# Optimization experiments

Hardware: AMD Instinct MI355X
Metric: run time of the kernel (lower is better)

Reference implementation:

```python
import jax, jax.numpy as jnp
import numpy as np

B, N, D, H = 4, 1024, 1024, 16
DH = D // H  # 64
FF = 4 * D   # 4096


def _layernorm(x, w, b, eps=1e-5):
    mu = jnp.mean(x, axis=-1, keepdims=True)
    var = jnp.var(x, axis=-1, keepdims=True)
    return (x - mu) * jax.lax.rsqrt(var + eps) * w + b


def setup_inputs() -> dict:
    key = jax.random.key(0)
    ks = jax.random.split(key, 8)
    s = 0.02
    return {
        "x": jax.random.normal(ks[0], (B, N, D), jnp.float32),
        "ln1_w": jnp.ones((D,), jnp.float32),
        "ln1_b": jnp.zeros((D,), jnp.float32),
        "qkv_w": jax.random.normal(ks[1], (3 * D, D), jnp.float32) * s,
        "qkv_b": jnp.zeros((3 * D,), jnp.float32),
        "proj_l_w": jax.random.normal(ks[2], (H, H), jnp.float32) * s,
        "proj_l_b": jnp.zeros((H,), jnp.float32),
        "proj_w_w": jax.random.normal(ks[3], (H, H), jnp.float32) * s,
        "proj_w_b": jnp.zeros((H,), jnp.float32),
        "out_w": jax.random.normal(ks[4], (D, D), jnp.float32) * s,
        "out_b": jnp.zeros((D,), jnp.float32),
        "gamma1": jnp.ones((D,), jnp.float32),
        "ln2_w": jnp.ones((D,), jnp.float32),
        "ln2_b": jnp.zeros((D,), jnp.float32),
        "fc1_w": jax.random.normal(ks[5], (FF, D), jnp.float32) * s,
        "fc1_b": jnp.zeros((FF,), jnp.float32),
        "fc2_w": jax.random.normal(ks[6], (D, FF), jnp.float32) * s,
        "fc2_b": jnp.zeros((D,), jnp.float32),
        "gamma2": jnp.ones((D,), jnp.float32),
    }


def reference(x, ln1_w, ln1_b, qkv_w, qkv_b, proj_l_w, proj_l_b, proj_w_w,
              proj_w_b, out_w, out_b, gamma1, ln2_w, ln2_b, fc1_w, fc1_b,
              fc2_w, fc2_b, gamma2):
    # ---- LayerScale(TalkingHeadAttention) branch ----
    h = _layernorm(x, ln1_w, ln1_b)
    qkv = h @ qkv_w.T + qkv_b                      # [B,N,3D]
    q, k, v = jnp.split(qkv, 3, axis=-1)
    # [B,N,D] -> [B,H,N,DH]
    reshape = lambda t: t.reshape(B, N, H, DH).transpose(0, 2, 1, 3)
    q, k, v = reshape(q), reshape(k), reshape(v)
    attn = jnp.einsum("bhid,bhjd->bhij", q, k) * (DH ** -0.5)
    # talking-heads mixing before softmax (Linear over head dim)
    attn = jnp.einsum("bhij,gh->bgij", attn, proj_l_w) + proj_l_b[None, :, None, None]
    attn = jax.nn.softmax(attn, axis=-1)
    # talking-heads mixing after softmax
    attn = jnp.einsum("bhij,gh->bgij", attn, proj_w_w) + proj_w_b[None, :, None, None]
    o = jnp.einsum("bhij,bhjd->bhid", attn, v)     # [B,H,N,DH]
    o = o.transpose(0, 2, 1, 3).reshape(B, N, D)
    o = o @ out_w.T + out_b
    x = x + gamma1 * o
    # ---- LayerScale(MLP) branch ----
    h = _layernorm(x, ln2_w, ln2_b)
    h = jax.nn.gelu(h @ fc1_w.T + fc1_b)
    h = h @ fc2_w.T + fc2_b
    return x + gamma2 * h
```

## Files before the change

kernel.cpp:

```cpp
#include <hip/hip_runtime.h>


typedef _Float16 f16x8 __attribute__((ext_vector_type(8)));
typedef _Float16 f16x4 __attribute__((ext_vector_type(4)));
typedef _Float16 f16x2 __attribute__((ext_vector_type(2)));
typedef float f32x4 __attribute__((ext_vector_type(4)));

#define B_ 4
#define N_ 1024
#define D_ 1024
#define H_ 16
#define DH_ 64
#define FF_ 4096
#define M_ (B_ * N_)

__device__ __forceinline__ float gelu_act(float x) {
  float z = 0.7978845608028654f * (x + 0.044715f * x * x * x);
  return x / (1.0f + __expf(-2.0f * z));
}

__device__ __forceinline__ void ld_lds16(const _Float16* g, _Float16* l) {
  __builtin_amdgcn_global_load_lds((const __attribute__((address_space(1))) void*)g,
                                   (__attribute__((address_space(3))) void*)l, 16, 0, 0);
}

__device__ __forceinline__ int swz8(int i) {
  return (((i >> 2) << 1) ^ (i & 3)) & 7;
}
__device__ __forceinline__ int lds_off(int p, int i, int j) {
  int ch = ((j >> 3) ^ swz8(i) ^ ((p >> 2) << 1)) & 7;
  return p * 1032 + i * 64 + (ch << 3) + (j & 7);
}

__global__ __launch_bounds__(256) void cast_all(
    const float* __restrict__ a0, _Float16* __restrict__ o0,
    const float* __restrict__ a1, _Float16* __restrict__ o1,
    const float* __restrict__ a2, _Float16* __restrict__ o2,
    const float* __restrict__ a3, _Float16* __restrict__ o3,
    const float* __restrict__ W1, const float* __restrict__ W2,
    _Float16* __restrict__ w1f, _Float16* __restrict__ w2f,
    float* __restrict__ bsum,
    const float* __restrict__ x, const float* __restrict__ ln_w,
    const float* __restrict__ ln_b, _Float16* __restrict__ hb) {
  int b = blockIdx.x, t = threadIdx.x;
  if (b >= 12289) {
    int row = b - 12289;
    const float* xr = x + (size_t)row * D_;
    float4 v = *(const float4*)(xr + t * 4);
    float s = v.x + v.y + v.z + v.w;
    float sq = v.x * v.x + v.y * v.y + v.z * v.z + v.w * v.w;
    #pragma unroll
    for (int off = 32; off > 0; off >>= 1) {
      s += __shfl_down(s, off);
      sq += __shfl_down(sq, off);
    }
    __shared__ float red[8];
    int wave = t >> 6, lane = t & 63;
    if (lane == 0) { red[wave] = s; red[4 + wave] = sq; }
    __syncthreads();
    float ts = red[0] + red[1] + red[2] + red[3];
    float tq = red[4] + red[5] + red[6] + red[7];
    float mean = ts * (1.0f / (float)D_);
    float var = tq * (1.0f / (float)D_) - mean * mean;
    float rs = rsqrtf(var + 1e-5f);
    float4 wv = *(const float4*)(ln_w + t * 4);
    float4 bv = *(const float4*)(ln_b + t * 4);
    f16x4 o;
    o[0] = (_Float16)((v.x - mean) * rs * wv.x + bv.x);
    o[1] = (_Float16)((v.y - mean) * rs * wv.y + bv.y);
    o[2] = (_Float16)((v.z - mean) * rs * wv.z + bv.z);
    o[3] = (_Float16)((v.w - mean) * rs * wv.w + bv.w);
    *(f16x4*)(hb + (size_t)row * D_ + t * 4) = o;
    return;
  }
  const float* in;
  _Float16* out;
  int base;
  if (b < 3072) { in = a0; out = o0; base = b; }
  else if (b < 4096) { in = a1; out = o1; base = b - 3072; }
  else if (b < 8192) { in = a2; out = o2; base = b - 4096; }
  else if (b < 12288) { in = a3; out = o3; base = b - 8192; }
  else {
    w1f[t] = (_Float16)W1[t];
    w2f[t] = (_Float16)W2[t];
    float4 z = {0.f, 0.f, 0.f, 0.f};
    #pragma unroll
    for (int r = 0; r < 4; r++) *(float4*)(bsum + t * 16 + r * 4) = z;
    return;
  }
  int i = (base * 256 + t) * 4;
  float4 v = *(const float4*)(in + i);
  f16x4 o;
  o[0] = (_Float16)v.x; o[1] = (_Float16)v.y; o[2] = (_Float16)v.z; o[3] = (_Float16)v.w;
  *(f16x4*)(out + i) = o;
}

__global__ __launch_bounds__(256) void ln_f16(const float* __restrict__ x,
                                              const float* __restrict__ w,
                                              const float* __restrict__ b,
                                              _Float16* __restrict__ out) {
  int row = blockIdx.x;
  int tid = threadIdx.x;
  const float* xr = x + (size_t)row * D_;
  float4 v = *(const float4*)(xr + tid * 4);
  float s = v.x + v.y + v.z + v.w;
  float sq = v.x * v.x + v.y * v.y + v.z * v.z + v.w * v.w;
  #pragma unroll
  for (int off = 32; off > 0; off >>= 1) {
    s += __shfl_down(s, off);
    sq += __shfl_down(sq, off);
  }
  __shared__ float red[8];
  int wave = tid >> 6, lane = tid & 63;
  if (lane == 0) { red[wave] = s; red[4 + wave] = sq; }
  __syncthreads();
  float ts = red[0] + red[1] + red[2] + red[3];
  float tq = red[4] + red[5] + red[6] + red[7];
  float mean = ts * (1.0f / (float)D_);
  float var = tq * (1.0f / (float)D_) - mean * mean;
  float rs = rsqrtf(var + 1e-5f);
  float4 wv = *(const float4*)(w + tid * 4);
  float4 bv = *(const float4*)(b + tid * 4);
  f16x4 o;
  o[0] = (_Float16)((v.x - mean) * rs * wv.x + bv.x);
  o[1] = (_Float16)((v.y - mean) * rs * wv.y + bv.y);
  o[2] = (_Float16)((v.z - mean) * rs * wv.z + bv.z);
  o[3] = (_Float16)((v.w - mean) * rs * wv.w + bv.w);
  *(f16x4*)(out + (size_t)row * D_ + tid * 4) = o;
}

template <int EPI, int BN, int OCC, int SWAPXY>
__global__ __launch_bounds__(256, OCC) void gemm_nt(
    const _Float16* __restrict__ A, const _Float16* __restrict__ W,
    const float* __restrict__ bias, int M, int N, int K,
    _Float16* __restrict__ outB, float* __restrict__ outF,
    const float* __restrict__ res, const float* __restrict__ gamma) {
  __shared__ _Float16 As[128 * 64];
  __shared__ _Float16 Bs[BN * 64];
  int tid = threadIdx.x;
  int wave = tid >> 6, lane = tid & 63;
  int quad = lane >> 4, l16 = lane & 15;
  int wm = wave >> 1, wn = wave & 1;
  int m0 = (SWAPXY ? blockIdx.x : blockIdx.y) * 128;
  int n0 = (SWAPXY ? blockIdx.y : blockIdx.x) * BN;
  int lrow = lane >> 3, lcol = (lane & 7) * 8;
  const int NI = (BN == 128) ? 4 : 2;
  const int WN = (BN == 128) ? 64 : 32;

  f32x4 zero = {0.f, 0.f, 0.f, 0.f};
  f32x4 acc[4][NI];
  #pragma unroll
  for (int i = 0; i < 4; i++)
    #pragma unroll
    for (int j = 0; j < NI; j++) acc[i][j] = zero;

  for (int k0 = 0; k0 < K; k0 += 64) {
    __syncthreads();
    #pragma unroll
    for (int c = 0; c < 4; c++) {
      int rb = c * 32 + wave * 8;
      ld_lds16(A + (size_t)(m0 + rb + lrow) * K + k0 + lcol, As + rb * 64);
      if (BN == 128 || c < 2)
        ld_lds16(W + (size_t)(n0 + rb + lrow) * K + k0 + lcol, Bs + rb * 64);
    }
    __syncthreads();
    #pragma unroll
    for (int ks = 0; ks < 2; ks++) {
      int kk = ks * 32 + quad * 8;
      f16x8 a[4], bfr[NI];
      #pragma unroll
      for (int i = 0; i < 4; i++) a[i] = *(const f16x8*)(As + (wm * 64 + i * 16 + l16) * 64 + kk);
      #pragma unroll
      for (int i = 0; i < NI; i++) bfr[i] = *(const f16x8*)(Bs + (wn * WN + i * 16 + l16) * 64 + kk);
      #pragma unroll
      for (int mi = 0; mi < 4; mi++)
        #pragma unroll
        for (int ni = 0; ni < NI; ni++)
          acc[mi][ni] = __builtin_amdgcn_mfma_f32_16x16x32_f16(a[mi], bfr[ni], acc[mi][ni], 0, 0, 0);
    }
  }

  #pragma unroll
  for (int mi = 0; mi < 4; mi++) {
    int grow_base = m0 + wm * 64 + mi * 16 + quad * 4;
    #pragma unroll
    for (int ni = 0; ni < NI; ni++) {
      int gcol = n0 + wn * WN + ni * 16 + l16;
      float bb = bias[gcol];
      float gm = (EPI == 1) ? gamma[gcol] : 0.f;
      #pragma unroll
      for (int r = 0; r < 4; r++) {
        size_t oi = (size_t)(grow_base + r) * N + gcol;
        float c = acc[mi][ni][r] + bb;
        if (EPI == 0) {
          outB[oi] = (_Float16)c;
        } else if (EPI == 1) {
          outF[oi] = res[oi] + gm * c;
        } else {
          outB[oi] = (_Float16)gelu_act(c);
        }
      }
    }
  }
}

#define GPH_OPEN()                                      \
  __builtin_amdgcn_sched_barrier(0);                    \
  __builtin_amdgcn_s_barrier();                         \
  asm volatile("s_waitcnt lgkmcnt(0)" ::: "memory");    \
  __builtin_amdgcn_sched_barrier(0);                    \
  __builtin_amdgcn_s_setprio(1)

#define GPH_CLOSE()                                     \
  __builtin_amdgcn_s_setprio(0);                        \
  __builtin_amdgcn_sched_barrier(0);                    \
  __builtin_amdgcn_s_barrier()

#define GPH_CLOSE_VM(n)                                 \
  __builtin_amdgcn_s_setprio(0);                        \
  __builtin_amdgcn_sched_barrier(0);                    \
  asm volatile("s_waitcnt vmcnt(" #n ")" ::: "memory"); \
  __builtin_amdgcn_s_barrier()

#define GMFMA(MB, NB)                                                         \
  _Pragma("unroll") for (int ks = 0; ks < 2; ks++)                            \
  _Pragma("unroll") for (int mi = 0; mi < 4; mi++)                            \
  _Pragma("unroll") for (int ni = 0; ni < 2; ni++)                            \
    acc[MB + mi][NB + ni] = __builtin_amdgcn_mfma_f32_16x16x32_f16(           \
        ar[mi][ks], br[NB + ni][ks], acc[MB + mi][NB + ni], 0, 0, 0)

#define LDA(buf, MB)                                            \
  _Pragma("unroll") for (int ks = 0; ks < 2; ks++)              \
  _Pragma("unroll") for (int mi = 0; mi < 4; mi++)              \
    ar[mi][ks] = rdf(&lds[buf][0][wm][0], MB + mi, ks)

#define LDB(buf, NB)                                            \
  _Pragma("unroll") for (int ks = 0; ks < 2; ks++)              \
  _Pragma("unroll") for (int ni = 0; ni < 2; ni++)              \
    br[NB + ni][ks] = rdf(&lds[buf][1][wn >> 1][0], fbB + NB + ni, ks)

template <int EPI>
__global__ __launch_bounds__(512, 2) void gemm_nt8(
    const _Float16* __restrict__ A, const _Float16* __restrict__ W,
    const float* __restrict__ bias, int M, int N, int K,
    _Float16* __restrict__ outB, _Float16* __restrict__ outB2) {
  __shared__ _Float16 lds[2][2][2][8192];
  const int tid = threadIdx.x;
  const int wv = tid >> 6, lane = tid & 63;
  const int quad = lane >> 4, l16 = lane & 15;
  const int wm = wv >> 2, wn = wv & 3;
  const int fbB = (wn & 1) * 4;
  const int wg = ((int)blockIdx.x & 7) * ((int)gridDim.x >> 3) + ((int)blockIdx.x >> 3);
  int split = 0, kt0 = 0, m0, n0;
  if (EPI == 3) {
    split = wg >> 6;
    int rem = wg & 63;
    m0 = (rem & 15) << 8;
    n0 = (rem >> 4) << 8;
    kt0 = split << 4;
  } else {
    m0 = (wg & 15) << 8;
    n0 = (wg >> 4) << 8;
  }
  const int gc = ((lane & 7) ^ (lane >> 3)) << 3;
  const int srow = wv * 8 + (lane >> 3);

  auto stageA = [&](int lt, int h) {
    const _Float16* g = A + (size_t)(m0 + h * 128 + srow) * K + (kt0 + lt) * 64 + gc;
    _Float16* l = &lds[lt & 1][0][h][wv * 512];
    ld_lds16(g, l);
    ld_lds16(g + (size_t)64 * K, l + 4096);
  };
  auto stageB = [&](int lt, int h) {
    const _Float16* g = W + (size_t)(n0 + h * 128 + srow) * K + (kt0 + lt) * 64 + gc;
    _Float16* l = &lds[lt & 1][1][h][wv * 512];
    ld_lds16(g, l);
    ld_lds16(g + (size_t)64 * K, l + 4096);
  };
  auto rdf = [&](const _Float16* base, int fi, int ks) -> f16x8 {
    int row = fi * 16 + l16;
    int pc = ((ks << 2) + quad) ^ (l16 & 7);
    return *(const f16x8*)(base + row * 64 + (pc << 3));
  };

  f32x4 acc[8][4];
  const f32x4 zero = {0.f, 0.f, 0.f, 0.f};
  #pragma unroll
  for (int i = 0; i < 8; i++)
    #pragma unroll
    for (int j = 0; j < 4; j++) acc[i][j] = zero;
  f16x8 ar[4][2], br[4][2];

  stageA(0, 0); stageA(0, 1); stageB(0, 0); stageB(0, 1);
  stageB(1, 0); stageB(1, 1);
  asm volatile("s_waitcnt vmcnt(4)" ::: "memory");
  __builtin_amdgcn_s_barrier();

  const int NT = 16;
  const int ITERS = NT >> 1;
  for (int it = 0; it < ITERS - 1; ++it) {
    const int t0 = it * 2;
    LDA(0, 0); LDB(0, 0); stageA(t0 + 1, 0);
    GPH_OPEN(); GMFMA(0, 0); GPH_CLOSE();
    LDB(0, 2); stageA(t0 + 1, 1);
    GPH_OPEN(); GMFMA(0, 2); GPH_CLOSE();
    LDA(0, 4); stageB(t0 + 2, 0);
    GPH_OPEN(); GMFMA(4, 0); GPH_CLOSE();
    stageB(t0 + 2, 1);
    GPH_OPEN(); GMFMA(4, 2); GPH_CLOSE_VM(4);
    LDA(1, 0); LDB(1, 0); stageA(t0 + 2, 0);
    GPH_OPEN(); GMFMA(0, 0); GPH_CLOSE();
    LDB(1, 2); stageA(t0 + 2, 1);
    GPH_OPEN(); GMFMA(0, 2); GPH_CLOSE();
    LDA(1, 4); stageB(t0 + 3, 0);
    GPH_OPEN(); GMFMA(4, 0); GPH_CLOSE();
    stageB(t0 + 3, 1);
    GPH_OPEN(); GMFMA(4, 2); GPH_CLOSE_VM(4);
  }
  {
    LDA(0, 0); LDB(0, 0); stageA(NT - 1, 0);
    GPH_OPEN(); GMFMA(0, 0); GPH_CLOSE();
    LDB(0, 2); stageA(NT - 1, 1);
    GPH_OPEN(); GMFMA(0, 2); GPH_CLOSE();
    LDA(0, 4);
    GPH_OPEN(); GMFMA(4, 0); GPH_CLOSE();
    GPH_OPEN(); GMFMA(4, 2); GPH_CLOSE_VM(0);
    LDA(1, 0); LDB(1, 0);
    GPH_OPEN(); GMFMA(0, 0); GPH_CLOSE();
    LDB(1, 2);
    GPH_OPEN(); GMFMA(0, 2); GPH_CLOSE();
    LDA(1, 4);
    GPH_OPEN(); GMFMA(4, 0); GPH_CLOSE();
    GPH_OPEN(); GMFMA(4, 2); GPH_CLOSE();
  }

  _Float16* po = outB;
  if (EPI == 3)
    po = (split < 2 ? outB : outB2) + (size_t)(split & 1) * ((size_t)M * N);
  #pragma unroll
  for (int mi = 0; mi < 8; mi++) {
    int grow = m0 + wm * 128 + mi * 16 + quad * 4;
    #pragma unroll
    for (int ni = 0; ni < 4; ni++) {
      int gcol = n0 + wn * 64 + ni * 16 + l16;
      float bb = (EPI == 3) ? 0.f : bias[gcol];
      #pragma unroll
      for (int r = 0; r < 4; r++) {
        size_t oi = (size_t)(grow + r) * N + gcol;
        float c = acc[mi][ni][r] + bb;
        po[oi] = (_Float16)(EPI == 2 ? gelu_act(c) : c);
      }
    }
  }
}

__global__ __launch_bounds__(256) void fc2_combine(
    const _Float16* __restrict__ p01, const _Float16* __restrict__ p23,
    const float* __restrict__ x1, const float* __restrict__ gamma,
    const float* __restrict__ bias, float* __restrict__ out) {
  const size_t idx = ((size_t)blockIdx.x * 256 + threadIdx.x) * 4;
  const int col = (int)(idx & (D_ - 1));
  const size_t soff = (size_t)M_ * D_;
  f16x4 a = *(const f16x4*)(p01 + idx);
  f16x4 b = *(const f16x4*)(p01 + soff + idx);
  f16x4 c = *(const f16x4*)(p23 + idx);
  f16x4 d = *(const f16x4*)(p23 + soff + idx);
  float4 xv = *(const float4*)(x1 + idx);
  float4 gv = *(const float4*)(gamma + col);
  float4 bv = *(const float4*)(bias + col);
  float4 o;
  o.x = xv.x + gv.x * ((float)a[0] + (float)b[0] + (float)c[0] + (float)d[0] + bv.x);
  o.y = xv.y + gv.y * ((float)a[1] + (float)b[1] + (float)c[1] + (float)d[1] + bv.y);
  o.z = xv.z + gv.z * ((float)a[2] + (float)b[2] + (float)c[2] + (float)d[2] + bv.z);
  o.w = xv.w + gv.w * ((float)a[3] + (float)b[3] + (float)c[3] + (float)d[3] + bv.w);
  *(float4*)(out + idx) = o;
}

__global__ __launch_bounds__(256) void transpose_v(const _Float16* __restrict__ qkv,
                                                   _Float16* __restrict__ vt,
                                                   const float* __restrict__ b2,
                                                   float* __restrict__ bsum) {
  int jt = blockIdx.x;
  int h = blockIdx.y;
  int b = blockIdx.z;
  __shared__ _Float16 tl[64][68];
  int tid = threadIdx.x;
  int j0 = jt * 64;
  #pragma unroll
  for (int k = 0; k < 16; k++) {
    int idx = k * 256 + tid;
    int jr = idx >> 6, dc = idx & 63;
    tl[jr][dc] = qkv[(size_t)(b * N_ + j0 + jr) * (3 * D_) + 2 * D_ + h * 64 + dc];
  }
  __syncthreads();
  #pragma unroll
  for (int k = 0; k < 16; k++) {
    int idx = k * 256 + tid;
    int dr = idx >> 6, jc = idx & 63;
    vt[(size_t)((b * H_ + h) * DH_ + dr) * N_ + j0 + jc] = tl[jc][dr];
  }
  int d = tid & 63, jq = tid >> 6;
  float s = 0.f;
  #pragma unroll
  for (int r = 0; r < 16; r++) s += (float)tl[jq * 16 + r][d];
  atomicAdd(&bsum[b * D_ + h * 64 + d], b2[h] * s);
}

__global__ __launch_bounds__(1024, 4) void attn_th(
    const _Float16* __restrict__ qkv, const _Float16* __restrict__ vt,
    const _Float16* __restrict__ w1f, const _Float16* __restrict__ w2f,
    const float* __restrict__ b1f, const float* __restrict__ bsum,
    _Float16* __restrict__ ob) {
  __shared__ __align__(16) _Float16 SP[2 * 16512];
  __shared__ float lsum[272];
  _Float16* Sp = SP;
  _Float16* Pp = SP + 16512;

  const int tid = threadIdx.x;
  const int wave = tid >> 6;
  const int lane = tid & 63;
  const int quad = lane >> 4, l16 = lane & 15;
  const int i0 = blockIdx.y * 16;
  const int b = blockIdx.x;
  const size_t bN = (size_t)b * N_;
  const f32x4 zero = {0.f, 0.f, 0.f, 0.f};

  f16x8 qf[2];
  #pragma unroll
  for (int ks = 0; ks < 2; ks++) {
    f16x8 q = *(const f16x8*)(qkv + (bN + i0 + l16) * 3072 + wave * 64 + ks * 32 + quad * 8);
    #pragma unroll
    for (int e = 0; e < 8; e++) q[e] = q[e] * (_Float16)0.125f;
    qf[ks] = q;
  }
  f16x4 w1a = *(const f16x4*)(w1f + l16 * 16 + quad * 4);
  float b1v = b1f[l16];
  f32x4 b1i = {b1v, b1v, b1v, b1v};

  const _Float16* vbase = vt + (size_t)((b * H_ + wave) * DH_ + l16) * N_ + quad * 8;

  f32x4 uacc[4];
  #pragma unroll
  for (int nt = 0; nt < 4; nt++) uacc[nt] = zero;
  float lacc = 0.f;

  f16x8 kcur[4][2];
  auto loadK = [&](int j0) {
    #pragma unroll
    for (int jb = 0; jb < 4; jb++) {
      const _Float16* kb = qkv + (bN + j0 + jb * 16 + l16) * 3072 + 1024 + wave * 64 + quad * 8;
      kcur[jb][0] = *(const f16x8*)kb;
      kcur[jb][1] = *(const f16x8*)(kb + 32);
    }
  };
  loadK(0);

  f16x8 vreg[4];

  for (int t = 0; t < 16; t++) {
    int j0 = t * 64;
    f32x4 sres[4];
    #pragma unroll
    for (int jb = 0; jb < 4; jb++) {
      f32x4 s = __builtin_amdgcn_mfma_f32_16x16x32_f16(kcur[jb][0], qf[0], zero, 0, 0, 0);
      sres[jb] = __builtin_amdgcn_mfma_f32_16x16x32_f16(kcur[jb][1], qf[1], s, 0, 0, 0);
    }
    #pragma unroll
    for (int jb = 0; jb < 4; jb++) {
      f16x4 sv;
      #pragma unroll
      for (int r = 0; r < 4; r++) sv[r] = (_Float16)sres[jb][r];
      *(f16x4*)(Sp + lds_off(wave, l16, jb * 16 + quad * 4)) = sv;
    }
    if (t < 15) loadK(j0 + 64);
    #pragma unroll
    for (int nt = 0; nt < 4; nt++)
      vreg[nt] = *(const f16x8*)(vbase + (size_t)(nt * 16) * N_ + j0);
    __syncthreads();
    #pragma unroll
    for (int cg = 0; cg < 4; cg++) {
      f16x4 sf;
      #pragma unroll
      for (int t4 = 0; t4 < 4; t4++)
        sf[t4] = Sp[lds_off(quad * 4 + t4, wave, cg * 16 + l16)];
      f32x4 a = __builtin_amdgcn_mfma_f32_16x16x16f16(sf, w1a, b1i, 0, 0, 0);
      f16x4 pv;
      #pragma unroll
      for (int r = 0; r < 4; r++) {
        float e = __expf(a[r]);
        lacc += e;
        pv[r] = (_Float16)e;
      }
      *(f16x4*)(Pp + lds_off(l16, wave, cg * 16 + quad * 4)) = pv;
    }
    __syncthreads();
    f16x8 pf0 = *(const f16x8*)(Pp + lds_off(wave, l16, quad * 8));
    f16x8 pf1 = *(const f16x8*)(Pp + lds_off(wave, l16, 32 + quad * 8));
    #pragma unroll
    for (int nt = 0; nt < 4; nt++)
      uacc[nt] = __builtin_amdgcn_mfma_f32_16x16x32_f16(vreg[nt], pf0, uacc[nt], 0, 0, 0);
    #pragma unroll
    for (int nt = 0; nt < 4; nt++) {
      f16x8 vf = *(const f16x8*)(vbase + (size_t)(nt * 16) * N_ + j0 + 32);
      uacc[nt] = __builtin_amdgcn_mfma_f32_16x16x32_f16(vf, pf1, uacc[nt], 0, 0, 0);
    }
  }

  lacc += __shfl_xor(lacc, 16);
  lacc += __shfl_xor(lacc, 32);
  __syncthreads();
  if (quad == 0) lsum[l16 * 17 + wave] = lacc;
  __syncthreads();
  float invl = 1.0f / lsum[wave * 17 + l16];

  _Float16* Uf = Sp;
  #pragma unroll
  for (int nt = 0; nt < 4; nt++) {
    f16x4 u;
    #pragma unroll
    for (int r = 0; r < 4; r++) u[r] = (_Float16)(uacc[nt][r] * invl);
    *(f16x4*)(Uf + wave * 1092 + l16 * 68 + nt * 16 + quad * 4) = u;
  }
  __syncthreads();

  f16x4 w2a = *(const f16x4*)(w2f + l16 * 16 + quad * 4);
  #pragma unroll
  for (int cg = 0; cg < 4; cg++) {
    f16x4 af;
    #pragma unroll
    for (int t4 = 0; t4 < 4; t4++)
      af[t4] = Uf[(quad * 4 + t4) * 1092 + wave * 68 + cg * 16 + l16];
    f32x4 o = __builtin_amdgcn_mfma_f32_16x16x16f16(af, w2a, zero, 0, 0, 0);
    f32x4 bs = *(const f32x4*)(bsum + b * D_ + l16 * 64 + cg * 16 + quad * 4);
    f16x4 ov;
    #pragma unroll
    for (int r = 0; r < 4; r++) ov[r] = (_Float16)(o[r] + bs[r]);
    *(f16x4*)(ob + (bN + i0 + wave) * D_ + l16 * 64 + cg * 16 + quad * 4) = ov;
  }
}

extern "C" void kernel_launch(void* const* d_in, const int* in_sizes, int n_in,
                              void* d_out, int out_size, void* d_ws, size_t ws_size,
                              hipStream_t stream) {
  const float* x      = (const float*)d_in[0];
  const float* ln1_w  = (const float*)d_in[1];
  const float* ln1_b  = (const float*)d_in[2];
  const float* qkv_w  = (const float*)d_in[3];
  const float* qkv_b  = (const float*)d_in[4];
  const float* plw    = (const float*)d_in[5];
  const float* plb    = (const float*)d_in[6];
  const float* pww    = (const float*)d_in[7];
  const float* pwb    = (const float*)d_in[8];
  const float* out_w  = (const float*)d_in[9];
  const float* out_b  = (const float*)d_in[10];
  const float* gamma1 = (const float*)d_in[11];
  const float* ln2_w  = (const float*)d_in[12];
  const float* ln2_b  = (const float*)d_in[13];
  const float* fc1_w  = (const float*)d_in[14];
  const float* fc1_b  = (const float*)d_in[15];
  const float* fc2_w  = (const float*)d_in[16];
  const float* fc2_b  = (const float*)d_in[17];
  const float* gamma2 = (const float*)d_in[18];
  float* out = (float*)d_out;

  char* ws = (char*)d_ws;
  _Float16* wq   = (_Float16*)(ws + 0);
  _Float16* wo   = (_Float16*)(ws + 6291456);
  _Float16* wf1  = (_Float16*)(ws + 8388608);
  _Float16* wf2  = (_Float16*)(ws + 16777216);
  float*    x1   = (float*)   (ws + 25165824);
  _Float16* ob   = (_Float16*)(ws + 41943040);
  _Float16* hb   = (_Float16*)(ws + 50331648);
  _Float16* qkvb = (_Float16*)(ws + 58720256);
  _Float16* vtb  = (_Float16*)(ws + 83886080);
  _Float16* fb   = (_Float16*)(ws + 58720256);
  _Float16* w1f  = (_Float16*)(ws + 25165824);
  _Float16* w2f  = (_Float16*)(ws + 25165824 + 512);
  float*    bsum = (float*)   (ws + 25165824 + 1024);
  _Float16* p01  = (_Float16*)(ws + 0);
  _Float16* p23  = (_Float16*)(ws + 41943040);
  if (ws_size < 92274688) return;

  cast_all<<<16385, 256, 0, stream>>>(qkv_w, wq, out_w, wo, fc1_w, wf1, fc2_w, wf2,
                                      plw, pww, w1f, w2f, bsum,
                                      x, ln1_w, ln1_b, hb);

  gemm_nt8<0><<<192, 512, 0, stream>>>(hb, wq, qkv_b, M_, 3 * D_, D_, qkvb, nullptr);
  transpose_v<<<dim3(16, 16, 4), 256, 0, stream>>>(qkvb, vtb, pwb, bsum);
  attn_th<<<dim3(4, 64), 1024, 0, stream>>>(qkvb, vtb, w1f, w2f, plb, bsum, ob);
  gemm_nt<1, 128, 3, 1><<<dim3(32, 8), 256, 0, stream>>>(ob, wo, out_b, M_, D_, D_, nullptr, x1, x, gamma1);

  ln_f16<<<4096, 256, 0, stream>>>(x1, ln2_w, ln2_b, hb);
  gemm_nt8<2><<<256, 512, 0, stream>>>(hb, wf1, fc1_b, M_, FF_, D_, fb, nullptr);
  gemm_nt8<3><<<256, 512, 0, stream>>>(fb, wf2, fc2_b, M_, D_, FF_, p01, p23);
  fc2_combine<<<4096, 256, 0, stream>>>(p01, p23, x1, gamma2, fc2_b, out);
}
```

Baseline: 411.2 us.

## Overlap out/fc1/fc2 weight casts with QKV GEMM via extra blocks

The fp32→fp16 casts of the output-projection, fc1 and fc2 weights move out of the upfront cast kernel. They become 768 extra blocks appended to the QKV GEMM launch, so those casts run alongside the GEMM tiles on otherwise idle compute units instead of serialising before it. The pre-pass now only casts the QKV weight, the talking-head weights and runs LayerNorm1. The cost is that the GEMM kernel gains a branch and extra parameters, and the cast blocks compete with the GEMM tiles for memory bandwidth.

New measurement: 412.0 us, median of 2. Within noise of the previous version (+0.2%).

```diff
diff --git a/kernel.cpp b/kernel.cpp
--- a/kernel.cpp
+++ b/kernel.cpp
@@ -34,17 +34,14 @@
 
 __global__ __launch_bounds__(256) void cast_all(
     const float* __restrict__ a0, _Float16* __restrict__ o0,
-    const float* __restrict__ a1, _Float16* __restrict__ o1,
-    const float* __restrict__ a2, _Float16* __restrict__ o2,
-    const float* __restrict__ a3, _Float16* __restrict__ o3,
     const float* __restrict__ W1, const float* __restrict__ W2,
     _Float16* __restrict__ w1f, _Float16* __restrict__ w2f,
     float* __restrict__ bsum,
     const float* __restrict__ x, const float* __restrict__ ln_w,
     const float* __restrict__ ln_b, _Float16* __restrict__ hb) {
   int b = blockIdx.x, t = threadIdx.x;
-  if (b >= 12289) {
-    int row = b - 12289;
+  if (b > 3072) {
+    int row = b - 3073;
     const float* xr = x + (size_t)row * D_;
     float4 v = *(const float4*)(xr + t * 4);
     float s = v.x + v.y + v.z + v.w;
@@ -73,14 +70,7 @@
     *(f16x4*)(hb + (size_t)row * D_ + t * 4) = o;
     return;
   }
-  const float* in;
-  _Float16* out;
-  int base;
-  if (b < 3072) { in = a0; out = o0; base = b; }
-  else if (b < 4096) { in = a1; out = o1; base = b - 3072; }
-  else if (b < 8192) { in = a2; out = o2; base = b - 4096; }
-  else if (b < 12288) { in = a3; out = o3; base = b - 8192; }
-  else {
+  if (b == 3072) {
     w1f[t] = (_Float16)W1[t];
     w2f[t] = (_Float16)W2[t];
     float4 z = {0.f, 0.f, 0.f, 0.f};
@@ -88,11 +78,11 @@
     for (int r = 0; r < 4; r++) *(float4*)(bsum + t * 16 + r * 4) = z;
     return;
   }
-  int i = (base * 256 + t) * 4;
-  float4 v = *(const float4*)(in + i);
+  int i = (b * 256 + t) * 4;
+  float4 v = *(const float4*)(a0 + i);
   f16x4 o;
   o[0] = (_Float16)v.x; o[1] = (_Float16)v.y; o[2] = (_Float16)v.z; o[3] = (_Float16)v.w;
-  *(f16x4*)(out + i) = o;
+  *(f16x4*)(o0 + i) = o;
 }
 
 __global__ __launch_bounds__(256) void ln_f16(const float* __restrict__ x,
@@ -243,14 +233,40 @@
 __global__ __launch_bounds__(512, 2) void gemm_nt8(
     const _Float16* __restrict__ A, const _Float16* __restrict__ W,
     const float* __restrict__ bias, int M, int N, int K,
-    _Float16* __restrict__ outB, _Float16* __restrict__ outB2) {
+    _Float16* __restrict__ outB, _Float16* __restrict__ outB2,
+    const float* __restrict__ c0, const float* __restrict__ c1,
+    const float* __restrict__ c2, _Float16* __restrict__ d0,
+    _Float16* __restrict__ d1, _Float16* __restrict__ d2) {
   __shared__ _Float16 lds[2][2][2][8192];
   const int tid = threadIdx.x;
+
+  if (EPI == 0 && (int)blockIdx.x >= 192) {
+    const int cb = (int)blockIdx.x - 192;
+    size_t g = ((size_t)cb * 512 + tid) * 4;
+    #pragma unroll
+    for (int sw = 0; sw < 6; sw++) {
+      size_t idx = g + (size_t)sw * 1572864;
+      const float* src;
+      _Float16* dst;
+      size_t off;
+      if (idx < 1048576) { src = c0; dst = d0; off = idx; }
+      else if (idx < 5242880) { src = c1; dst = d1; off = idx - 1048576; }
+      else { src = c2; dst = d2; off = idx - 5242880; }
+      float4 v = *(const float4*)(src + off);
+      f16x4 o;
+      o[0] = (_Float16)v.x; o[1] = (_Float16)v.y;
+      o[2] = (_Float16)v.z; o[3] = (_Float16)v.w;
+      *(f16x4*)(dst + off) = o;
+    }
+    return;
+  }
+
   const int wv = tid >> 6, lane = tid & 63;
   const int quad = lane >> 4, l16 = lane & 15;
   const int wm = wv >> 2, wn = wv & 3;
   const int fbB = (wn & 1) * 4;
-  const int wg = ((int)blockIdx.x & 7) * ((int)gridDim.x >> 3) + ((int)blockIdx.x >> 3);
+  const int GB = (EPI == 0) ? 192 : 256;
+  const int wg = ((int)blockIdx.x & 7) * (GB >> 3) + ((int)blockIdx.x >> 3);
   int split = 0, kt0 = 0, m0, n0;
   if (EPI == 3) {
     split = wg >> 6;
@@ -581,17 +597,19 @@
   _Float16* p23  = (_Float16*)(ws + 41943040);
   if (ws_size < 92274688) return;
 
-  cast_all<<<16385, 256, 0, stream>>>(qkv_w, wq, out_w, wo, fc1_w, wf1, fc2_w, wf2,
-                                      plw, pww, w1f, w2f, bsum,
-                                      x, ln1_w, ln1_b, hb);
-
-  gemm_nt8<0><<<192, 512, 0, stream>>>(hb, wq, qkv_b, M_, 3 * D_, D_, qkvb, nullptr);
+  cast_all<<<7169, 256, 0, stream>>>(qkv_w, wq, plw, pww, w1f, w2f, bsum,
+                                     x, ln1_w, ln1_b, hb);
+
+  gemm_nt8<0><<<960, 512, 0, stream>>>(hb, wq, qkv_b, M_, 3 * D_, D_, qkvb, nullptr,
+                                       out_w, fc1_w, fc2_w, wo, wf1, wf2);
   transpose_v<<<dim3(16, 16, 4), 256, 0, stream>>>(qkvb, vtb, pwb, bsum);
   attn_th<<<dim3(4, 64), 1024, 0, stream>>>(qkvb, vtb, w1f, w2f, plb, bsum, ob);
   gemm_nt<1, 128, 3, 1><<<dim3(32, 8), 256, 0, stream>>>(ob, wo, out_b, M_, D_, D_, nullptr, x1, x, gamma1);
 
   ln_f16<<<4096, 256, 0, stream>>>(x1, ln2_w, ln2_b, hb);
-  gemm_nt8<2><<<256, 512, 0, stream>>>(hb, wf1, fc1_b, M_, FF_, D_, fb, nullptr);
-  gemm_nt8<3><<<256, 512, 0, stream>>>(fb, wf2, fc2_b, M_, D_, FF_, p01, p23);
+  gemm_nt8<2><<<256, 512, 0, stream>>>(hb, wf1, fc1_b, M_, FF_, D_, fb, nullptr,
+                                       nullptr, nullptr, nullptr, nullptr, nullptr, nullptr);
+  gemm_nt8<3><<<256, 512, 0, stream>>>(fb, wf2, fc2_b, M_, D_, FF_, p01, p23,
+                                       nullptr, nullptr, nullptr, nullptr, nullptr, nullptr);
   fc2_combine<<<4096, 256, 0, stream>>>(p01, p23, x1, gamma2, fc2_b, out);
 }
```
